# Kernel optimization log

Measured on AMD Instinct MI355X. Metric: run time of the kernel, lower is better.

## Reference

```python
import jax, jax.numpy as jnp
import numpy as np

N_NODES = 50000
NNZ = 800000
HYPER_DIM = 128
N_LAYERS = 2
LEAKY = 0.2
LN_EPS = 1e-5


def setup_inputs() -> dict:
    key = jax.random.key(0)
    k1, k2, k3, k4 = jax.random.split(key, 4)
    return {
        "ego_embeddings": jax.random.normal(k1, (N_NODES, HYPER_DIM), dtype=jnp.float32),
        "adj_vals": jax.random.uniform(k2, (NNZ,), dtype=jnp.float32),
        "ln_gamma": jnp.ones((N_LAYERS, HYPER_DIM), dtype=jnp.float32),
        "ln_beta": jnp.zeros((N_LAYERS, HYPER_DIM), dtype=jnp.float32),
        "adj_rows": jax.random.randint(k3, (NNZ,), 0, N_NODES, dtype=jnp.int32),
        "adj_cols": jax.random.randint(k4, (NNZ,), 0, N_NODES, dtype=jnp.int32),
        "n_users": 25000,
    }


def _spmm(rows, cols, vals, x, n_out):
    # y = A @ x for sparse A in COO (rows, cols, vals): gather + segment-sum
    return jax.ops.segment_sum(vals[:, None] * x[cols], rows, num_segments=n_out)


def _layer_norm(x, gamma, beta):
    mu = jnp.mean(x, axis=-1, keepdims=True)
    var = jnp.mean(jnp.square(x - mu), axis=-1, keepdims=True)
    return (x - mu) * jax.lax.rsqrt(var + LN_EPS) * gamma + beta


def reference(ego_embeddings, adj_vals, ln_gamma, ln_beta, adj_rows, adj_cols, n_users):
    res = ego_embeddings
    embs = ego_embeddings
    for k in range(N_LAYERS):
        # adj.T @ embs  (rows of A^T are cols of A)
        ht = _spmm(adj_cols, adj_rows, adj_vals, embs, N_NODES)
        # adj @ (adj.T @ embs)
        h = _spmm(adj_rows, adj_cols, adj_vals, ht, N_NODES)
        if k != N_LAYERS - 1:
            h = jnp.where(h >= 0, h, LEAKY * h)  # LeakyReLU
        embs = _layer_norm(h, ln_gamma[k], ln_beta[k]) + res
    user_emb = embs[:n_users]
    item_emb = embs[n_users:]
    return (user_emb, item_emb)
```

## Files before the change

### kernel.cpp

```cpp
#include <hip/hip_runtime.h>
#include <hip/hip_bf16.h>

#define HD 128
#define G 32
#define RLOG 5
#define PR 8
#define LEAKY 0.2f
#define LN_EPS 1e-5f
#define TILE 4096

__device__ __forceinline__ unsigned short bfr(float f) {
    unsigned int b = __float_as_uint(f);
    return (unsigned short)((b + 0x7fffu + ((b >> 16) & 1u)) >> 16);
}
__device__ __forceinline__ float blo(unsigned int u) { return __uint_as_float(u << 16); }
__device__ __forceinline__ float bhi(unsigned int u) { return __uint_as_float(u & 0xffff0000u); }

__global__ __launch_bounds__(256) void f32_to_bf16(
    const float* __restrict__ x, unsigned short* __restrict__ y, int n4) {
    int i = blockIdx.x * 256 + threadIdx.x;
    if (i >= n4) return;
    float4 f = ((const float4*)x)[i];
    ushort4 u;
    u.x = bfr(f.x); u.y = bfr(f.y); u.z = bfr(f.z); u.w = bfr(f.w);
    ((ushort4*)y)[i] = u;
}

__global__ __launch_bounds__(1024) void histo_lds(
    const int* __restrict__ rows, const int* __restrict__ cols,
    int* __restrict__ cnt_r, int* __restrict__ cnt_c, int nnz, int n) {
    __shared__ unsigned ldsR[3136], ldsC[3136];
    int p = blockIdx.x & (PR - 1);
    int g = blockIdx.x >> 3;
    int per = (n + PR - 1) / PR;
    int lo = p * per;
    int hi = min(lo + per, n);
    int nb = hi - lo;
    int nw = (nb + 1) >> 1;
    for (int j = threadIdx.x; j < nw; j += 1024) { ldsR[j] = 0u; ldsC[j] = 0u; }
    __syncthreads();

    int chunk = (nnz + G - 1) / G;
    int beg = g * chunk;
    int end = min(beg + chunk, nnz);
    for (int i = beg + threadIdx.x; i < end; i += 1024) {
        unsigned obr = (unsigned)(rows[i] - lo);
        unsigned obc = (unsigned)(cols[i] - lo);
        if (obr < (unsigned)nb) atomicAdd(&ldsR[obr >> 1], 1u << ((obr & 1) * 16));
        if (obc < (unsigned)nb) atomicAdd(&ldsC[obc >> 1], 1u << ((obc & 1) * 16));
    }
    __syncthreads();
    for (int j = threadIdx.x; j < nb; j += 1024) {
        int sh = (j & 1) * 16;
        cnt_r[(size_t)g * n + lo + j] = (ldsR[j >> 1] >> sh) & 0xffffu;
        cnt_c[(size_t)g * n + lo + j] = (ldsC[j >> 1] >> sh) & 0xffffu;
    }
}

__global__ __launch_bounds__(256) void scan_sum(
    const int* __restrict__ cnt, int* __restrict__ partials, int n, int tiles) {
    int a = blockIdx.y;
    const int* base = cnt + (size_t)a * n * G;
    int M = n * G;
    int t0 = blockIdx.x * TILE + threadIdx.x * 16;
    int s = 0;
    #pragma unroll
    for (int j = 0; j < 16; ++j) {
        int p = t0 + j;
        if (p < M) s += base[(p & (G - 1)) * n + (p >> RLOG)];
    }
    #pragma unroll
    for (int off = 32; off; off >>= 1) s += __shfl_xor(s, off);
    __shared__ int ws[4];
    int lane = threadIdx.x & 63, wid = threadIdx.x >> 6;
    if (lane == 0) ws[wid] = s;
    __syncthreads();
    if (threadIdx.x == 0)
        partials[a * tiles + blockIdx.x] = ws[0] + ws[1] + ws[2] + ws[3];
}

__global__ __launch_bounds__(128) void scan_partials(
    int* __restrict__ partials, int tiles,
    int* __restrict__ rp_r, int* __restrict__ rp_c, int n, int nnz) {
    int wid = threadIdx.x >> 6, lane = threadIdx.x & 63;
    int* p = partials + wid * tiles;
    int v[8], s = 0;
    #pragma unroll
    for (int j = 0; j < 8; ++j) {
        int idx = lane * 8 + j;
        v[j] = (idx < tiles) ? p[idx] : 0;
        s += v[j];
    }
    int incl = s;
    #pragma unroll
    for (int off = 1; off < 64; off <<= 1) {
        int t = __shfl_up(incl, off);
        if (lane >= off) incl += t;
    }
    int excl = incl - s;
    #pragma unroll
    for (int j = 0; j < 8; ++j) {
        int idx = lane * 8 + j;
        if (idx < tiles) p[idx] = excl;
        excl += v[j];
    }
    if (lane == 0) (wid ? rp_c : rp_r)[n] = nnz;
}

__global__ __launch_bounds__(256) void scan_apply(
    int* __restrict__ cnt, const int* __restrict__ partials,
    int* __restrict__ rp_r, int* __restrict__ rp_c, int n, int tiles) {
    int a = blockIdx.y;
    int* base = cnt + (size_t)a * n * G;
    int* rp = a ? rp_c : rp_r;
    int M = n * G;
    int t0 = blockIdx.x * TILE + threadIdx.x * 16;
    int v[16];
    int s = 0;
    #pragma unroll
    for (int j = 0; j < 16; ++j) {
        int p = t0 + j;
        v[j] = (p < M) ? base[(p & (G - 1)) * n + (p >> RLOG)] : 0;
        s += v[j];
    }
    int lane = threadIdx.x & 63, wid = threadIdx.x >> 6;
    int incl = s;
    #pragma unroll
    for (int off = 1; off < 64; off <<= 1) {
        int t = __shfl_up(incl, off);
        if (lane >= off) incl += t;
    }
    __shared__ int wsum[4], woff[4];
    if (lane == 63) wsum[wid] = incl;
    __syncthreads();
    if (threadIdx.x == 0) {
        int run = 0;
        #pragma unroll
        for (int w = 0; w < 4; ++w) { woff[w] = run; run += wsum[w]; }
    }
    __syncthreads();
    int excl = partials[a * tiles + blockIdx.x] + woff[wid] + incl - s;
    #pragma unroll
    for (int j = 0; j < 16; ++j) {
        int p = t0 + j;
        if (p < M) {
            int b = p >> RLOG, r = p & (G - 1);
            base[r * n + b] = excl;
            if (r == 0) rp[b] = excl;
            excl += v[j];
        }
    }
}

__global__ __launch_bounds__(1024) void fill_lds(
    const int* __restrict__ rows, const int* __restrict__ cols,
    const float* __restrict__ vals,
    const int* __restrict__ base_r, const int* __restrict__ base_c,
    unsigned* __restrict__ ent_r, unsigned* __restrict__ ent_c, int nnz, int n) {
    __shared__ unsigned ldsR[3136], ldsC[3136];
    int p = blockIdx.x & (PR - 1);
    int g = blockIdx.x >> 3;
    int per = (n + PR - 1) / PR;
    int lo = p * per;
    int hi = min(lo + per, n);
    int nb = hi - lo;
    int nw = (nb + 1) >> 1;
    for (int j = threadIdx.x; j < nw; j += 1024) { ldsR[j] = 0u; ldsC[j] = 0u; }
    __syncthreads();

    int chunk = (nnz + G - 1) / G;
    int beg = g * chunk;
    int end = min(beg + chunk, nnz);
    for (int i = beg + threadIdx.x; i < end; i += 1024) {
        int ro = rows[i], co = cols[i];
        unsigned obr = (unsigned)(ro - lo);
        unsigned obc = (unsigned)(co - lo);
        if ((obr < (unsigned)nb) | (obc < (unsigned)nb)) {
            unsigned vb = (unsigned)bfr(vals[i]) << 16;
            if (obr < (unsigned)nb) {
                int sh = (obr & 1) * 16;
                unsigned old = atomicAdd(&ldsR[obr >> 1], 1u << sh);
                int rank = (old >> sh) & 0xffffu;
                ent_r[base_r[(size_t)g * n + ro] + rank] = vb | (unsigned)co;
            }
            if (obc < (unsigned)nb) {
                int sh = (obc & 1) * 16;
                unsigned old = atomicAdd(&ldsC[obc >> 1], 1u << sh);
                int rank = (old >> sh) & 0xffffu;
                ent_c[base_c[(size_t)g * n + co] + rank] = vb | (unsigned)ro;
            }
        }
    }
}

__global__ __launch_bounds__(256) void spmm_bf(
    const unsigned short* __restrict__ x, const int* __restrict__ rp,
    const unsigned* __restrict__ ent,
    const float* __restrict__ res, const float* __restrict__ gamma,
    const float* __restrict__ beta,
    unsigned short* __restrict__ out_bf, float* __restrict__ out_f32,
    int n, int post) {
    int wid = threadIdx.x >> 6, lane = threadIdx.x & 63;
    int row = blockIdx.x * 4 + wid;
    if (row >= n) return;
    int quarter = lane >> 4, q = lane & 15;
    int beg = rp[row], end = rp[row + 1];
    float acc[8];
    #pragma unroll
    for (int k = 0; k < 8; ++k) acc[k] = 0.f;

    int i = beg + quarter;
    for (; i + 12 < end; i += 16) {
        unsigned e0 = ent[i], e1 = ent[i + 4], e2 = ent[i + 8], e3 = ent[i + 12];
        uint4 u0 = ((const uint4*)(x + (size_t)(e0 & 0xffffu) * HD))[q];
        uint4 u1 = ((const uint4*)(x + (size_t)(e1 & 0xffffu) * HD))[q];
        uint4 u2 = ((const uint4*)(x + (size_t)(e2 & 0xffffu) * HD))[q];
        uint4 u3 = ((const uint4*)(x + (size_t)(e3 & 0xffffu) * HD))[q];
        float v0 = bhi(e0), v1 = bhi(e1), v2 = bhi(e2), v3 = bhi(e3);
        acc[0] += v0 * blo(u0.x) + v1 * blo(u1.x);
        acc[1] += v0 * bhi(u0.x) + v1 * bhi(u1.x);
        acc[2] += v0 * blo(u0.y) + v1 * blo(u1.y);
        acc[3] += v0 * bhi(u0.y) + v1 * bhi(u1.y);
        acc[4] += v0 * blo(u0.z) + v1 * blo(u1.z);
        acc[5] += v0 * bhi(u0.z) + v1 * bhi(u1.z);
        acc[6] += v0 * blo(u0.w) + v1 * blo(u1.w);
        acc[7] += v0 * bhi(u0.w) + v1 * bhi(u1.w);
        acc[0] += v2 * blo(u2.x) + v3 * blo(u3.x);
        acc[1] += v2 * bhi(u2.x) + v3 * bhi(u3.x);
        acc[2] += v2 * blo(u2.y) + v3 * blo(u3.y);
        acc[3] += v2 * bhi(u2.y) + v3 * bhi(u3.y);
        acc[4] += v2 * blo(u2.z) + v3 * blo(u3.z);
        acc[5] += v2 * bhi(u2.z) + v3 * bhi(u3.z);
        acc[6] += v2 * blo(u2.w) + v3 * blo(u3.w);
        acc[7] += v2 * bhi(u2.w) + v3 * bhi(u3.w);
    }
    for (; i < end; i += 4) {
        unsigned e0 = ent[i];
        uint4 u0 = ((const uint4*)(x + (size_t)(e0 & 0xffffu) * HD))[q];
        float v0 = bhi(e0);
        acc[0] += v0 * blo(u0.x);
        acc[1] += v0 * bhi(u0.x);
        acc[2] += v0 * blo(u0.y);
        acc[3] += v0 * bhi(u0.y);
        acc[4] += v0 * blo(u0.z);
        acc[5] += v0 * bhi(u0.z);
        acc[6] += v0 * blo(u0.w);
        acc[7] += v0 * bhi(u0.w);
    }
    #pragma unroll
    for (int k = 0; k < 8; ++k) {
        acc[k] += __shfl_xor(acc[k], 16);
        acc[k] += __shfl_xor(acc[k], 32);
    }
    if (quarter != 0) return;

    if (post == 0) {
        uint4 s;
        s.x = (unsigned)bfr(acc[0]) | ((unsigned)bfr(acc[1]) << 16);
        s.y = (unsigned)bfr(acc[2]) | ((unsigned)bfr(acc[3]) << 16);
        s.z = (unsigned)bfr(acc[4]) | ((unsigned)bfr(acc[5]) << 16);
        s.w = (unsigned)bfr(acc[6]) | ((unsigned)bfr(acc[7]) << 16);
        ((uint4*)(out_bf + (size_t)row * HD))[q] = s;
        return;
    }
    if (post == 1) {
        #pragma unroll
        for (int k = 0; k < 8; ++k) acc[k] = acc[k] >= 0.f ? acc[k] : LEAKY * acc[k];
    }
    float t = 0.f;
    #pragma unroll
    for (int k = 0; k < 8; ++k) t += acc[k];
    #pragma unroll
    for (int off = 1; off < 16; off <<= 1) t += __shfl_xor(t, off);
    float mu = t * (1.f / HD);
    float d[8], vs = 0.f;
    #pragma unroll
    for (int k = 0; k < 8; ++k) { d[k] = acc[k] - mu; vs += d[k] * d[k]; }
    #pragma unroll
    for (int off = 1; off < 16; off <<= 1) vs += __shfl_xor(vs, off);
    float inv = rsqrtf(vs * (1.f / HD) + LN_EPS);

    float4 g0 = ((const float4*)gamma)[2 * q], g1 = ((const float4*)gamma)[2 * q + 1];
    float4 b0 = ((const float4*)beta)[2 * q],  b1 = ((const float4*)beta)[2 * q + 1];
    float4 r0 = ((const float4*)(res + (size_t)row * HD))[2 * q];
    float4 r1 = ((const float4*)(res + (size_t)row * HD))[2 * q + 1];
    float o[8];
    o[0] = d[0] * inv * g0.x + b0.x + r0.x;
    o[1] = d[1] * inv * g0.y + b0.y + r0.y;
    o[2] = d[2] * inv * g0.z + b0.z + r0.z;
    o[3] = d[3] * inv * g0.w + b0.w + r0.w;
    o[4] = d[4] * inv * g1.x + b1.x + r1.x;
    o[5] = d[5] * inv * g1.y + b1.y + r1.y;
    o[6] = d[6] * inv * g1.z + b1.z + r1.z;
    o[7] = d[7] * inv * g1.w + b1.w + r1.w;
    if (post == 1) {
        uint4 s;
        s.x = (unsigned)bfr(o[0]) | ((unsigned)bfr(o[1]) << 16);
        s.y = (unsigned)bfr(o[2]) | ((unsigned)bfr(o[3]) << 16);
        s.z = (unsigned)bfr(o[4]) | ((unsigned)bfr(o[5]) << 16);
        s.w = (unsigned)bfr(o[6]) | ((unsigned)bfr(o[7]) << 16);
        ((uint4*)(out_bf + (size_t)row * HD))[q] = s;
    } else {
        float4 s0 = {o[0], o[1], o[2], o[3]};
        float4 s1 = {o[4], o[5], o[6], o[7]};
        ((float4*)(out_f32 + (size_t)row * HD))[2 * q] = s0;
        ((float4*)(out_f32 + (size_t)row * HD))[2 * q + 1] = s1;
    }
}

extern "C" void kernel_launch(void* const* d_in, const int* in_sizes, int n_in,
                              void* d_out, int out_size, void* d_ws, size_t ws_size,
                              hipStream_t stream) {
    const float* ego   = (const float*)d_in[0];
    const float* vals  = (const float*)d_in[1];
    const float* gamma = (const float*)d_in[2];
    const float* beta  = (const float*)d_in[3];
    const int*   rows  = (const int*)d_in[4];
    const int*   cols  = (const int*)d_in[5];

    const int N   = in_sizes[0] / HD;
    const int NNZ = in_sizes[1];

    float* out = (float*)d_out;
    char* w = (char*)d_ws;
    unsigned short* ego_bf = (unsigned short*)w; w += (size_t)N * HD * 2;
    unsigned short* bufA   = (unsigned short*)w; w += (size_t)N * HD * 2;
    unsigned short* bufB   = (unsigned short*)w; w += (size_t)N * HD * 2;
    int*  rp_r = (int*)w;  w += (size_t)(N + 4) * 4;
    int*  rp_c = (int*)w;  w += (size_t)(N + 4) * 4;
    unsigned* ent_r = (unsigned*)w; w += (size_t)NNZ * 4;
    unsigned* ent_c = (unsigned*)w; w += (size_t)NNZ * 4;
    int*  partials = (int*)w; w += 8192;

    int* cnt_r  = (int*)bufB;
    int* cnt_c  = cnt_r + (size_t)G * N;

    const int tiles = (N * G + TILE - 1) / TILE;

    f32_to_bf16<<<(N * HD / 4 + 255) / 256, 256, 0, stream>>>(ego, ego_bf, N * HD / 4);
    histo_lds<<<G * PR, 1024, 0, stream>>>(rows, cols, cnt_r, cnt_c, NNZ, N);
    scan_sum<<<dim3(tiles, 2), 256, 0, stream>>>(cnt_r, partials, N, tiles);
    scan_partials<<<1, 128, 0, stream>>>(partials, tiles, rp_r, rp_c, N, NNZ);
    scan_apply<<<dim3(tiles, 2), 256, 0, stream>>>(cnt_r, partials, rp_r, rp_c, N, tiles);
    fill_lds<<<G * PR, 1024, 0, stream>>>(rows, cols, vals, cnt_r, cnt_c,
                                          ent_r, ent_c, NNZ, N);

    const int sblocks = (N + 3) / 4;

    spmm_bf<<<sblocks, 256, 0, stream>>>(ego_bf, rp_c, ent_c,
                                         nullptr, nullptr, nullptr, bufA, nullptr, N, 0);
    spmm_bf<<<sblocks, 256, 0, stream>>>(bufA, rp_r, ent_r,
                                         ego, gamma, beta, bufB, nullptr, N, 1);
    spmm_bf<<<sblocks, 256, 0, stream>>>(bufB, rp_c, ent_c,
                                         nullptr, nullptr, nullptr, bufA, nullptr, N, 0);
    spmm_bf<<<sblocks, 256, 0, stream>>>(bufA, rp_r, ent_r,
                                         ego, gamma + HD, beta + HD, nullptr, out, N, 2);
}
```

Measured before the change: 294.4 us.

## Replace per-row histogram CSR build with two-pass bucket partition sort

Swaps the CSR/CSC construction for a two-level radix partition. The first pass scatters entries into 1024-row buckets using coarse per-block LDS counters and a small scan. The second pass is one 1024-thread block per bucket that does a local counting sort and writes row pointers. This drops the large G×N count array and its multi-kernel scan, at the cost of a staging buffer of 8-byte entries and an extra read/write pass over the nonzeros. Row order inside a bucket now depends on atomic order, so accumulation order can vary between runs.

```diff
diff --git a/kernel.cpp b/kernel.cpp
--- a/kernel.cpp
+++ b/kernel.cpp
@@ -2,12 +2,9 @@
 #include <hip/hip_bf16.h>
 
 #define HD 128
-#define G 32
-#define RLOG 5
-#define PR 8
+#define PB 256
 #define LEAKY 0.2f
 #define LN_EPS 1e-5f
-#define TILE 4096
 
 __device__ __forceinline__ unsigned short bfr(float f) {
     unsigned int b = __float_as_uint(f);
@@ -26,69 +23,36 @@
     ((ushort4*)y)[i] = u;
 }
 
-__global__ __launch_bounds__(1024) void histo_lds(
+
+__global__ __launch_bounds__(256) void part_count(
     const int* __restrict__ rows, const int* __restrict__ cols,
-    int* __restrict__ cnt_r, int* __restrict__ cnt_c, int nnz, int n) {
-    __shared__ unsigned ldsR[3136], ldsC[3136];
-    int p = blockIdx.x & (PR - 1);
-    int g = blockIdx.x >> 3;
-    int per = (n + PR - 1) / PR;
-    int lo = p * per;
-    int hi = min(lo + per, n);
-    int nb = hi - lo;
-    int nw = (nb + 1) >> 1;
-    for (int j = threadIdx.x; j < nw; j += 1024) { ldsR[j] = 0u; ldsC[j] = 0u; }
-    __syncthreads();
-
-    int chunk = (nnz + G - 1) / G;
-    int beg = g * chunk;
+    int* __restrict__ counts, int nnz) {
+    __shared__ int cR[64], cC[64];
+    if (threadIdx.x < 64) { cR[threadIdx.x] = 0; cC[threadIdx.x] = 0; }
+    __syncthreads();
+    int chunk = (nnz + PB - 1) / PB;
+    int beg = blockIdx.x * chunk;
     int end = min(beg + chunk, nnz);
-    for (int i = beg + threadIdx.x; i < end; i += 1024) {
-        unsigned obr = (unsigned)(rows[i] - lo);
-        unsigned obc = (unsigned)(cols[i] - lo);
-        if (obr < (unsigned)nb) atomicAdd(&ldsR[obr >> 1], 1u << ((obr & 1) * 16));
-        if (obc < (unsigned)nb) atomicAdd(&ldsC[obc >> 1], 1u << ((obc & 1) * 16));
-    }
-    __syncthreads();
-    for (int j = threadIdx.x; j < nb; j += 1024) {
-        int sh = (j & 1) * 16;
-        cnt_r[(size_t)g * n + lo + j] = (ldsR[j >> 1] >> sh) & 0xffffu;
-        cnt_c[(size_t)g * n + lo + j] = (ldsC[j >> 1] >> sh) & 0xffffu;
-    }
-}
-
-__global__ __launch_bounds__(256) void scan_sum(
-    const int* __restrict__ cnt, int* __restrict__ partials, int n, int tiles) {
-    int a = blockIdx.y;
-    const int* base = cnt + (size_t)a * n * G;
-    int M = n * G;
-    int t0 = blockIdx.x * TILE + threadIdx.x * 16;
-    int s = 0;
-    #pragma unroll
-    for (int j = 0; j < 16; ++j) {
-        int p = t0 + j;
-        if (p < M) s += base[(p & (G - 1)) * n + (p >> RLOG)];
-    }
-    #pragma unroll
-    for (int off = 32; off; off >>= 1) s += __shfl_xor(s, off);
-    __shared__ int ws[4];
-    int lane = threadIdx.x & 63, wid = threadIdx.x >> 6;
-    if (lane == 0) ws[wid] = s;
-    __syncthreads();
-    if (threadIdx.x == 0)
-        partials[a * tiles + blockIdx.x] = ws[0] + ws[1] + ws[2] + ws[3];
-}
-
-__global__ __launch_bounds__(128) void scan_partials(
-    int* __restrict__ partials, int tiles,
-    int* __restrict__ rp_r, int* __restrict__ rp_c, int n, int nnz) {
-    int wid = threadIdx.x >> 6, lane = threadIdx.x & 63;
-    int* p = partials + wid * tiles;
-    int v[8], s = 0;
-    #pragma unroll
-    for (int j = 0; j < 8; ++j) {
-        int idx = lane * 8 + j;
-        v[j] = (idx < tiles) ? p[idx] : 0;
+    for (int i = beg + threadIdx.x; i < end; i += 256) {
+        atomicAdd(&cR[rows[i] >> 10], 1);
+        atomicAdd(&cC[cols[i] >> 10], 1);
+    }
+    __syncthreads();
+    if (threadIdx.x < 64) {
+        counts[(size_t)blockIdx.x * 64 + threadIdx.x] = cR[threadIdx.x];
+        counts[(size_t)PB * 64 + blockIdx.x * 64 + threadIdx.x] = cC[threadIdx.x];
+    }
+}
+
+__global__ __launch_bounds__(64) void part_off(
+    int* __restrict__ counts, int* __restrict__ totals) {
+    int bkt = blockIdx.x, dir = blockIdx.y, lane = threadIdx.x;
+    int* p = counts + (size_t)dir * PB * 64;
+    int v[4], s = 0;
+    #pragma unroll
+    for (int j = 0; j < 4; ++j) {
+        int blk = lane * 4 + j;
+        v[j] = p[(size_t)blk * 64 + bkt];
         s += v[j];
     }
     int incl = s;
@@ -99,97 +63,100 @@
     }
     int excl = incl - s;
     #pragma unroll
-    for (int j = 0; j < 8; ++j) {
-        int idx = lane * 8 + j;
-        if (idx < tiles) p[idx] = excl;
+    for (int j = 0; j < 4; ++j) {
+        int blk = lane * 4 + j;
+        p[(size_t)blk * 64 + bkt] = excl;
         excl += v[j];
     }
-    if (lane == 0) (wid ? rp_c : rp_r)[n] = nnz;
-}
-
-__global__ __launch_bounds__(256) void scan_apply(
-    int* __restrict__ cnt, const int* __restrict__ partials,
-    int* __restrict__ rp_r, int* __restrict__ rp_c, int n, int tiles) {
-    int a = blockIdx.y;
-    int* base = cnt + (size_t)a * n * G;
-    int* rp = a ? rp_c : rp_r;
-    int M = n * G;
-    int t0 = blockIdx.x * TILE + threadIdx.x * 16;
-    int v[16];
-    int s = 0;
-    #pragma unroll
-    for (int j = 0; j < 16; ++j) {
-        int p = t0 + j;
-        v[j] = (p < M) ? base[(p & (G - 1)) * n + (p >> RLOG)] : 0;
-        s += v[j];
-    }
-    int lane = threadIdx.x & 63, wid = threadIdx.x >> 6;
-    int incl = s;
+    if (lane == 63) totals[dir * 64 + bkt] = incl;
+}
+
+__global__ __launch_bounds__(128) void base_scan(
+    const int* __restrict__ totals, int* __restrict__ bases,
+    int* __restrict__ rp_r, int* __restrict__ rp_c, int nbk, int n, int nnz) {
+    int dir = threadIdx.x >> 6, lane = threadIdx.x & 63;
+    int v = (lane < nbk) ? totals[dir * 64 + lane] : 0;
+    int incl = v;
     #pragma unroll
     for (int off = 1; off < 64; off <<= 1) {
         int t = __shfl_up(incl, off);
         if (lane >= off) incl += t;
     }
-    __shared__ int wsum[4], woff[4];
+    bases[dir * 64 + lane] = incl - v;
+    if (lane == 0) (dir ? rp_c : rp_r)[n] = nnz;
+}
+
+__global__ __launch_bounds__(256) void part_scatter(
+    const int* __restrict__ rows, const int* __restrict__ cols,
+    const float* __restrict__ vals,
+    const int* __restrict__ counts, const int* __restrict__ bases,
+    uint2* __restrict__ stg_r, uint2* __restrict__ stg_c, int nnz) {
+    __shared__ int cR[64], cC[64], wbR[64], wbC[64];
+    if (threadIdx.x < 64) {
+        cR[threadIdx.x] = 0; cC[threadIdx.x] = 0;
+        wbR[threadIdx.x] = bases[threadIdx.x] +
+            counts[(size_t)blockIdx.x * 64 + threadIdx.x];
+        wbC[threadIdx.x] = bases[64 + threadIdx.x] +
+            counts[(size_t)PB * 64 + blockIdx.x * 64 + threadIdx.x];
+    }
+    __syncthreads();
+    int chunk = (nnz + PB - 1) / PB;
+    int beg = blockIdx.x * chunk;
+    int end = min(beg + chunk, nnz);
+    for (int i = beg + threadIdx.x; i < end; i += 256) {
+        int ro = rows[i], co = cols[i];
+        unsigned vb = (unsigned)bfr(vals[i]) << 16;
+        int rk = atomicAdd(&cR[ro >> 10], 1);
+        stg_r[wbR[ro >> 10] + rk] = make_uint2(vb | (unsigned)co, (unsigned)ro);
+        int ck = atomicAdd(&cC[co >> 10], 1);
+        stg_c[wbC[co >> 10] + ck] = make_uint2(vb | (unsigned)ro, (unsigned)co);
+    }
+}
+
+__global__ __launch_bounds__(1024) void bucket_build(
+    const uint2* __restrict__ stg_r, const uint2* __restrict__ stg_c,
+    const int* __restrict__ totals, const int* __restrict__ bases,
+    unsigned* __restrict__ ent_r, unsigned* __restrict__ ent_c,
+    int* __restrict__ rp_r, int* __restrict__ rp_c, int n) {
+    __shared__ int cnt[1024];
+    __shared__ int wsum[16], woff[16];
+    int bkt = blockIdx.x, dir = blockIdx.y;
+    const uint2* stg = dir ? stg_c : stg_r;
+    unsigned* ent = dir ? ent_c : ent_r;
+    int* rp = dir ? rp_c : rp_r;
+    int base = bases[dir * 64 + bkt];
+    int total = totals[dir * 64 + bkt];
+    int lo = bkt << 10;
+    int nb = min(1024, n - lo);
+    cnt[threadIdx.x] = 0;
+    __syncthreads();
+    for (int i = threadIdx.x; i < total; i += 1024)
+        atomicAdd(&cnt[(int)stg[base + i].y - lo], 1);
+    __syncthreads();
+    int lane = threadIdx.x & 63, wid = threadIdx.x >> 6;
+    int v = cnt[threadIdx.x];
+    int incl = v;
+    #pragma unroll
+    for (int off = 1; off < 64; off <<= 1) {
+        int t = __shfl_up(incl, off);
+        if (lane >= off) incl += t;
+    }
     if (lane == 63) wsum[wid] = incl;
     __syncthreads();
     if (threadIdx.x == 0) {
         int run = 0;
         #pragma unroll
-        for (int w = 0; w < 4; ++w) { woff[w] = run; run += wsum[w]; }
-    }
-    __syncthreads();
-    int excl = partials[a * tiles + blockIdx.x] + woff[wid] + incl - s;
-    #pragma unroll
-    for (int j = 0; j < 16; ++j) {
-        int p = t0 + j;
-        if (p < M) {
-            int b = p >> RLOG, r = p & (G - 1);
-            base[r * n + b] = excl;
-            if (r == 0) rp[b] = excl;
-            excl += v[j];
-        }
-    }
-}
-
-__global__ __launch_bounds__(1024) void fill_lds(
-    const int* __restrict__ rows, const int* __restrict__ cols,
-    const float* __restrict__ vals,
-    const int* __restrict__ base_r, const int* __restrict__ base_c,
-    unsigned* __restrict__ ent_r, unsigned* __restrict__ ent_c, int nnz, int n) {
-    __shared__ unsigned ldsR[3136], ldsC[3136];
-    int p = blockIdx.x & (PR - 1);
-    int g = blockIdx.x >> 3;
-    int per = (n + PR - 1) / PR;
-    int lo = p * per;
-    int hi = min(lo + per, n);
-    int nb = hi - lo;
-    int nw = (nb + 1) >> 1;
-    for (int j = threadIdx.x; j < nw; j += 1024) { ldsR[j] = 0u; ldsC[j] = 0u; }
-    __syncthreads();
-
-    int chunk = (nnz + G - 1) / G;
-    int beg = g * chunk;
-    int end = min(beg + chunk, nnz);
-    for (int i = beg + threadIdx.x; i < end; i += 1024) {
-        int ro = rows[i], co = cols[i];
-        unsigned obr = (unsigned)(ro - lo);
-        unsigned obc = (unsigned)(co - lo);
-        if ((obr < (unsigned)nb) | (obc < (unsigned)nb)) {
-            unsigned vb = (unsigned)bfr(vals[i]) << 16;
-            if (obr < (unsigned)nb) {
-                int sh = (obr & 1) * 16;
-                unsigned old = atomicAdd(&ldsR[obr >> 1], 1u << sh);
-                int rank = (old >> sh) & 0xffffu;
-                ent_r[base_r[(size_t)g * n + ro] + rank] = vb | (unsigned)co;
-            }
-            if (obc < (unsigned)nb) {
-                int sh = (obc & 1) * 16;
-                unsigned old = atomicAdd(&ldsC[obc >> 1], 1u << sh);
-                int rank = (old >> sh) & 0xffffu;
-                ent_c[base_c[(size_t)g * n + co] + rank] = vb | (unsigned)ro;
-            }
-        }
+        for (int w = 0; w < 16; ++w) { woff[w] = run; run += wsum[w]; }
+    }
+    __syncthreads();
+    int excl = woff[wid] + incl - v;
+    if (threadIdx.x < nb) rp[lo + threadIdx.x] = base + excl;
+    cnt[threadIdx.x] = excl;
+    __syncthreads();
+    for (int i = threadIdx.x; i < total; i += 1024) {
+        uint2 e = stg[base + i];
+        int pos = atomicAdd(&cnt[(int)e.y - lo], 1);
+        ent[base + pos] = e.x;
     }
 }
 
@@ -320,6 +287,7 @@
 
     const int N   = in_sizes[0] / HD;
     const int NNZ = in_sizes[1];
+    const int NBK = (N + 1023) >> 10;
 
     float* out = (float*)d_out;
     char* w = (char*)d_ws;
@@ -330,20 +298,21 @@
     int*  rp_c = (int*)w;  w += (size_t)(N + 4) * 4;
     unsigned* ent_r = (unsigned*)w; w += (size_t)NNZ * 4;
     unsigned* ent_c = (unsigned*)w; w += (size_t)NNZ * 4;
-    int*  partials = (int*)w; w += 8192;
-
-    int* cnt_r  = (int*)bufB;
-    int* cnt_c  = cnt_r + (size_t)G * N;
-
-    const int tiles = (N * G + TILE - 1) / TILE;
+    int* counts = (int*)w; w += (size_t)2 * PB * 64 * 4;
+    int* totals = (int*)w; w += 128 * 4;
+    int* bases  = (int*)w; w += 128 * 4;
+
+    uint2* stg_r = (uint2*)bufB;
+    uint2* stg_c = stg_r + NNZ;
 
     f32_to_bf16<<<(N * HD / 4 + 255) / 256, 256, 0, stream>>>(ego, ego_bf, N * HD / 4);
-    histo_lds<<<G * PR, 1024, 0, stream>>>(rows, cols, cnt_r, cnt_c, NNZ, N);
-    scan_sum<<<dim3(tiles, 2), 256, 0, stream>>>(cnt_r, partials, N, tiles);
-    scan_partials<<<1, 128, 0, stream>>>(partials, tiles, rp_r, rp_c, N, NNZ);
-    scan_apply<<<dim3(tiles, 2), 256, 0, stream>>>(cnt_r, partials, rp_r, rp_c, N, tiles);
-    fill_lds<<<G * PR, 1024, 0, stream>>>(rows, cols, vals, cnt_r, cnt_c,
-                                          ent_r, ent_c, NNZ, N);
+    part_count<<<PB, 256, 0, stream>>>(rows, cols, counts, NNZ);
+    part_off<<<dim3(NBK, 2), 64, 0, stream>>>(counts, totals);
+    base_scan<<<1, 128, 0, stream>>>(totals, bases, rp_r, rp_c, NBK, N, NNZ);
+    part_scatter<<<PB, 256, 0, stream>>>(rows, cols, vals, counts, bases,
+                                         stg_r, stg_c, NNZ);
+    bucket_build<<<dim3(NBK, 2), 1024, 0, stream>>>(stg_r, stg_c, totals, bases,
+                                                    ent_r, ent_c, rp_r, rp_c, N);
 
     const int sblocks = (N + 3) / 4;
 
```

Measured after the change: 267.2 us, median of 2. -9.2%, faster.
